# Kernel tuning notes

Measured on AMD Instinct MI355X. Metric: run time of the kernel, lower is better.

## Reference

```python
import jax, jax.numpy as jnp
import numpy as np

EPS = 1e-4
SLOPE = 0.01
NFFT = 512
HOP = 256
CH_IN = 8
CH_H = 64
FREQ = NFFT // 2 + 1
LEN = 48000
BATCH = 2


def hann(n):
    return (0.5 - 0.5 * jnp.cos(2.0 * np.pi * jnp.arange(n) / n)).astype(jnp.float32)


def stft(x):
    # x: (B, C, L) -> (B, 2, C, F, T)  (torch.stft: center=True, reflect pad, hann window)
    pad = NFFT // 2
    xp = jnp.pad(x, ((0, 0), (0, 0), (pad, pad)), mode='reflect')
    T = 1 + x.shape[-1] // HOP
    idx = jnp.arange(T)[:, None] * HOP + jnp.arange(NFFT)[None, :]
    frames = xp[..., idx] * hann(NFFT)            # (B, C, T, NFFT)
    sp = jnp.fft.rfft(frames, axis=-1)            # (B, C, T, F)
    sp = jnp.swapaxes(sp, -1, -2)                 # (B, C, F, T)
    return jnp.stack([sp.real, sp.imag], axis=1).astype(jnp.float32)


def istft(re, im, length):
    # re, im: (B, C, F, T) -> (B, C, length) via windowed overlap-add
    sp = jnp.swapaxes(re + 1j * im, -1, -2)       # (B, C, T, F)
    win = hann(NFFT)
    frames = jnp.fft.irfft(sp, n=NFFT, axis=-1) * win
    pad = NFFT // 2
    total = length + 2 * pad
    T = frames.shape[-2]
    idx = jnp.arange(T)[:, None] * HOP + jnp.arange(NFFT)[None, :]
    out = jnp.zeros(frames.shape[:-2] + (total,), frames.dtype).at[..., idx].add(frames)
    wsum = jnp.zeros((total,), frames.dtype).at[idx].add(jnp.broadcast_to(win ** 2, (T, NFFT)))
    return (out / jnp.maximum(wsum, 1e-11))[..., pad:pad + length]


def conv2d(x, w, b, padT=0):
    y = jax.lax.conv_general_dilated(x, w, (1, 1), ((0, 0), (padT, padT)),
                                     dimension_numbers=('NCHW', 'OIHW', 'NCHW'))
    return y + b[None, :, None, None]


def cconv(x, w, b, padT=0):
    # complex conv on x: (B,2,C,F,T); w: (2,O,C,kf,kt) = [W_real, W_imag]; b: (2,O)
    r = conv2d(x[:, 0], w[0], b[0], padT) - conv2d(x[:, 1], w[1], b[1], padT)
    i = conv2d(x[:, 1], w[0], b[0], padT) + conv2d(x[:, 0], w[1], b[1], padT)
    return jnp.stack([r, i], axis=1)


def modExp(x, m=5.0):
    em = float(np.exp(m))
    return jnp.where(x > m, (x - m) * em + em, jnp.exp(jnp.minimum(x, m)))


def cExp(t):
    e = modExp(t[:, 0]) - 1.0
    return jnp.stack([e * jnp.cos(t[:, 1] - 1.0), e * jnp.sin(t[:, 1] - 1.0)], axis=1)


def snap(x):
    x = jnp.where((x >= 0) & (x < EPS), EPS, x)
    return jnp.where((x < 0) & (x > -EPS), -EPS, x)


def cLog(t):
    re = snap(t[:, 0])
    im = snap(t[:, 1])
    real = jnp.log(jnp.sqrt(im ** 2 + re ** 2 + EPS ** 2) + 1.0)
    imag = jnp.arctan(im / re)
    return jnp.stack([real, imag], axis=1)


def cMul(a, b):
    r = a[:, 0] * b[:, 0] - a[:, 1] * b[:, 1]
    i = a[:, 0] * b[:, 1] + a[:, 1] * b[:, 0]
    return jnp.stack([r, i], axis=1)


def trelu(t, tr, b):
    nr = t[:, 0] * tr[0, 0] + t[:, 1] * tr[0, 1] + b[0]
    ni = t[:, 0] * tr[1, 0] + t[:, 1] * tr[1, 1] + b[1]
    return jnp.stack([jax.nn.leaky_relu(nr, SLOPE), jax.nn.leaky_relu(ni, SLOPE)], axis=1)


def tgate(t, tr, b):
    gr = jax.nn.sigmoid(t[:, 0] * tr[0, 0] + t[:, 1] * tr[0, 1] + b[0])
    gi = jax.nn.sigmoid(t[:, 0] * tr[1, 0] + t[:, 1] * tr[1, 1] + b[1])
    return gr * gi + (1.0 - gr) * (1.0 - gi)


def perm(t):
    return jnp.transpose(t, (0, 1, 3, 2, 4))


def lrelu(x):
    return jax.nn.leaky_relu(x, SLOPE)


def forward(mix, fs_w, fs_b, fr_w, fr_b, c1r_w, c1r_b, c1i_w, c1i_b, c1_w, c1_b,
            c2r_w, c2r_b, c2i_w, c2i_b, c2_w, c2_b, a1_t, a1_b, a2_t, a2_b,
            c3r_w, c3r_b, c3i_w, c3i_b, c3_w, c3_b, c4r_w, c4r_b, c4i_w, c4i_b,
            c4_w, c4_b, a3_t, a3_b, a4_t, a4_b, f1_w, f1_b, f2_w, f2_b,
            cw_w, cw_b, fg_t, fg_b):
    ts = perm(cconv(perm(stft(mix)), fs_w, fs_b))      # (B,2,C,F,T)
    # ---- branch 1 ----
    tl = cLog(ts)
    tl = jnp.stack([conv2d(tl[:, 0], c1r_w, c1r_b), conv2d(tl[:, 1], c1r_w, c1r_b)], 1)
    tl = jnp.stack([conv2d(lrelu(tl[:, 0]), c1i_w, c1i_b), conv2d(tl[:, 1], c1i_w, c1i_b)], 1)
    tl = trelu(cExp(tl), a1_t, a1_b)
    t = cconv(tl, c1_w, c1_b)
    tl = cLog(t)
    tl = jnp.stack([conv2d(tl[:, 0], c2r_w, c2r_b, 7), conv2d(tl[:, 1], c2r_w, c2r_b, 7)], 1)[..., :-7]
    tl = jnp.stack([conv2d(lrelu(tl[:, 0]), c2i_w, c2i_b, 7), conv2d(tl[:, 1], c2i_w, c2i_b, 7)], 1)[..., :-7]
    tl = cExp(tl)
    tl1 = tl
    tc = cconv(ts, c2_w, c2_b, 7)[..., :-7]
    t = trelu(cMul(tl, tc), a2_t, a2_b)
    t = cconv(t, f1_w, f1_b)
    td1 = jnp.sum(ts - t, axis=2, keepdims=True) / ts.shape[2]
    # ---- branch 2 ----
    tl = cLog(ts)
    tl = jnp.stack([conv2d(tl[:, 0], c3r_w, c3r_b), conv2d(tl[:, 1], c3r_w, c3r_b)], 1)
    tl = jnp.stack([conv2d(lrelu(tl[:, 0]), c3i_w, c3i_b), conv2d(tl[:, 1], c3i_w, c3i_b)], 1)
    tl = trelu(cExp(tl), a3_t, a3_b)
    t = cconv(tl, c3_w, c3_b)
    tl = cLog(t)
    tl = jnp.stack([conv2d(tl[:, 0], c4r_w, c4r_b, 7), conv2d(tl[:, 1], c4r_w, c4r_b, 7)], 1)[..., :-7]
    tl = jnp.stack([conv2d(lrelu(tl[:, 0]), c4i_w, c4i_b, 7), conv2d(tl[:, 1], c4i_w, c4i_b, 7)], 1)[..., :-7]
    tl = cExp(tl)
    tc = cconv(ts, c4_w, c4_b, 7)[..., :-7]
    t = trelu(cMul(tl, tc), a4_t, a4_b)
    td2 = cconv(t, f2_w, f2_b)                         # (B,2,1,F,T)
    # ---- fuse ----
    f = cconv(jnp.concatenate([tl1, tl], axis=2), cw_w, cw_b)
    f = tgate(f, fg_t, fg_b)[:, None]                  # (B,1,1,F,T)
    td = td1 * f + td2 * (1.0 - f)
    t = perm(cconv(perm(td), fr_w, fr_b))
    return istft(t[:, 0], t[:, 1], LEN)                # (B,1,LEN)


def setup_inputs() -> dict:
    ks = iter(jax.random.split(jax.random.key(0), 64))
    def rn(shape, s=0.05):
        return s * jax.random.normal(next(ks), shape, jnp.float32)
    F, C, H = FREQ, CH_IN, CH_H
    inp = {
        'mix': jax.random.normal(next(ks), (BATCH, C, LEN), jnp.float32),
        'fs_w': rn((2, F, F, 1, 1)), 'fs_b': rn((2, F), 0.01),
        'fr_w': rn((2, F, F, 1, 1)), 'fr_b': rn((2, F), 0.01),
        'c1r_w': rn((H, C, 1, 1)), 'c1r_b': rn((H,), 0.01),
        'c1i_w': rn((H, H, 1, 1)), 'c1i_b': rn((H,), 0.01),
        'c1_w': rn((2, H, H, 1, 1)), 'c1_b': rn((2, H), 0.01),
        'c2r_w': rn((H, H, 1, 8)), 'c2r_b': rn((H,), 0.01),
        'c2i_w': rn((H, H, 1, 8)), 'c2i_b': rn((H,), 0.01),
        'c2_w': rn((2, H, C, 1, 8)), 'c2_b': rn((2, H), 0.01),
        'a1_t': rn((2, 2, H, F, 1), 0.5), 'a1_b': rn((2, H, F, 1), 0.5),
        'a2_t': rn((2, 2, H, F, 1), 0.5), 'a2_b': rn((2, H, F, 1), 0.5),
        'c3r_w': rn((H, C, 1, 1)), 'c3r_b': rn((H,), 0.01),
        'c3i_w': rn((H, H, 1, 1)), 'c3i_b': rn((H,), 0.01),
        'c3_w': rn((2, H, H, 1, 1)), 'c3_b': rn((2, H), 0.01),
        'c4r_w': rn((H, H, 1, 8)), 'c4r_b': rn((H,), 0.01),
        'c4i_w': rn((H, H, 1, 8)), 'c4i_b': rn((H,), 0.01),
        'c4_w': rn((2, H, C, 1, 8)), 'c4_b': rn((2, H), 0.01),
        'a3_t': rn((2, 2, H, F, 1), 0.5), 'a3_b': rn((2, H, F, 1), 0.5),
        'a4_t': rn((2, 2, H, F, 1), 0.5), 'a4_b': rn((2, H, F, 1), 0.5),
        'f1_w': rn((2, C, H, 1, 1)), 'f1_b': rn((2, C), 0.01),
        'f2_w': rn((2, 1, H, 1, 1)), 'f2_b': rn((2, 1), 0.01),
        'cw_w': rn((2, 1, 2 * H, 1, 1)), 'cw_b': rn((2, 1), 0.01),
        'fg_t': rn((2, 2, 1, F, 1), 0.5), 'fg_b': rn((2, 1, F, 1), 0.5),
    }
    return inp


def reference(mix, fs_w, fs_b, fr_w, fr_b, c1r_w, c1r_b, c1i_w, c1i_b, c1_w, c1_b,
              c2r_w, c2r_b, c2i_w, c2i_b, c2_w, c2_b, a1_t, a1_b, a2_t, a2_b,
              c3r_w, c3r_b, c3i_w, c3i_b, c3_w, c3_b, c4r_w, c4r_b, c4i_w, c4i_b,
              c4_w, c4_b, a3_t, a3_b, a4_t, a4_b, f1_w, f1_b, f2_w, f2_b,
              cw_w, cw_b, fg_t, fg_b):
    return forward(mix, fs_w, fs_b, fr_w, fr_b, c1r_w, c1r_b, c1i_w, c1i_b, c1_w, c1_b,
                   c2r_w, c2r_b, c2i_w, c2i_b, c2_w, c2_b, a1_t, a1_b, a2_t, a2_b,
                   c3r_w, c3r_b, c3i_w, c3i_b, c3_w, c3_b, c4r_w, c4r_b, c4i_w, c4i_b,
                   c4_w, c4_b, a3_t, a3_b, a4_t, a4_b, f1_w, f1_b, f2_w, f2_b,
                   cw_w, cw_b, fg_t, fg_b)
```

## Files before the change

### kernel.cpp

```cpp
#include <hip/hip_runtime.h>
#include <math.h>

#define DEV __device__ __forceinline__

constexpr int B_   = 2;
constexpr int C_IN = 8;
constexpr int H_   = 64;
constexpr int F_   = 257;
constexpr int T_   = 188;
constexpr int TW   = 96;
constexpr int NFFT = 512;
constexpr int HOP  = 256;
constexpr int LEN  = 48000;
constexpr int PADL = 256;
constexpr int FT   = F_ * T_;
constexpr float EPSV  = 1e-4f;
constexpr float SLOPEV = 0.01f;
constexpr float PI2 = 6.283185307179586f;

typedef __attribute__((ext_vector_type(8))) short short8;
typedef __attribute__((ext_vector_type(4))) short short4v;
typedef __attribute__((ext_vector_type(4))) float float4v;

DEV float lrelu_f(float x) { return x > 0.f ? x : SLOPEV * x; }
DEV float snap_f(float x) {
  if (x >= 0.f && x < EPSV) return EPSV;
  if (x < 0.f && x > -EPSV) return -EPSV;
  return x;
}
DEV float fast_atan(float z) {
  float az = fabsf(z);
  float u = az > 1.f ? __builtin_amdgcn_rcpf(az) : az;
  float u2 = u * u;
  float p = -0.01172120f;
  p = p * u2 + 0.05265332f;
  p = p * u2 - 0.11643287f;
  p = p * u2 + 0.19354346f;
  p = p * u2 - 0.33262347f;
  p = p * u2 + 0.99997726f;
  float r = p * u;
  if (az > 1.f) r = 1.5707963267948966f - r;
  return z < 0.f ? -r : r;
}
DEV float modexp_f(float x) {
  const float em = 148.4131591025766f;
  return x > 5.f ? (x - 5.f) * em + em : __expf(x);
}
DEV void cexp_f(float tr, float ti, float& er, float& ei) {
  float e = modexp_f(tr) - 1.f;
  float a = ti - 1.f;
  er = e * __cosf(a); ei = e * __sinf(a);
}
DEV float sigmoid_f(float x) { return 1.f / (1.f + __expf(-x)); }

DEV short f2bf(float x) {
  unsigned u = __float_as_uint(x);
  unsigned r = (u + 0x7fffu + ((u >> 16) & 1u)) >> 16;
  return (short)r;
}
DEV float bf2f(short h) {
  return __uint_as_float(((unsigned)(unsigned short)h) << 16);
}
DEV unsigned pack_hl(float v) {
  short hi = f2bf(v);
  short lo = f2bf(v - bf2f(hi));
  return ((unsigned)(unsigned short)hi << 16) | (unsigned)(unsigned short)lo;
}

__global__ void k_mixsplit(const float* __restrict__ x, short* __restrict__ hi,
                           short* __restrict__ lo) {
  int i = blockIdx.x * 256 + threadIdx.x;
  if (i >= B_ * C_IN * LEN / 4) return;
  float4v v = *(const float4v*)(x + (size_t)i * 4);
  short4v h, l;
  #pragma unroll
  for (int j = 0; j < 4; ++j) {
    h[j] = f2bf(v[j]);
    l[j] = f2bf(v[j] - bf2f(h[j]));
  }
  *(short4v*)(hi + (size_t)i * 4) = h;
  *(short4v*)(lo + (size_t)i * 4) = l;
}

__global__ __launch_bounds__(256) void k_mixdft(const float* __restrict__ W,
                                                short* __restrict__ wpk) {
  constexpr int MT = 33;
  __shared__ float wr_s[F_], wi_s[F_];
  int m = blockIdx.x;
  int k = blockIdx.y * 256 + threadIdx.x;
  int po = m >= F_;
  int fo = m - po * F_;
  if (m < 2 * F_) {
    for (int i = threadIdx.x; i < F_; i += 256) {
      wr_s[i] = W[fo * F_ + i];
      wi_s[i] = W[F_ * F_ + fo * F_ + i];
    }
  }
  __syncthreads();
  float val = 0.f;
  if (m < 2 * F_) {
    float sd, cd;
    sincosf((PI2 / NFFT) * k, &sd, &cd);
    float cs = 1.f, sn = 0.f;
    float ar = 0.f, ai = 0.f;
    for (int fi = 0; fi < F_; ++fi) {
      float wrv = wr_s[fi], wiv = wi_s[fi];
      ar += wrv * cs + wiv * sn;
      ai += wiv * cs - wrv * sn;
      float t2 = cs * cd - sn * sd;
      sn = sn * cd + cs * sd;
      cs = t2;
    }
    float win = 0.5f - 0.5f * cd;
    val = (po ? ai : ar) * win;
  }
  int mtg = m >> 4;
  int lane2 = ((k >> 3) & 3) * 16 + (m & 15);
  int s = k >> 5;
  int j = k & 7;
  short hi = f2bf(val);
  short lo = f2bf(val - bf2f(hi));
  wpk[(((0 * 16 + s) * MT + mtg) * 64 + lane2) * 8 + j] = hi;
  wpk[(((16 + s) * MT + mtg) * 64 + lane2) * 8 + j] = lo;
}

constexpr int TWS = 48;
__global__ __launch_bounds__(256) void k_stftmix(
    const short* __restrict__ mhi, const short* __restrict__ mlo,
    const short* __restrict__ wpk, const float* __restrict__ bias,
    float* __restrict__ Y) {
  constexpr int PITCH = 136;
  constexpr int MT = 33;
  __shared__ short xs_hi[TWS * PITCH];
  __shared__ short xs_lo[TWS * PITCH];
  int mg = blockIdx.x;
  int bc = blockIdx.y;
  int b = bc >> 3, c = bc & 7;
  int t0 = blockIdx.z * TWS;
  int tid = threadIdx.x;
  int lane = tid & 63;
  int wv = __builtin_amdgcn_readfirstlane(tid >> 6);
  int mtg = mg * 4 + wv;
  int q = lane >> 4;
  int n = lane & 15;

  const short* mh_ = mhi + (size_t)(b * C_IN + c) * LEN;
  const short* ml_ = mlo + (size_t)(b * C_IN + c) * LEN;

  float4v acc[3];
  #pragma unroll
  for (int nt = 0; nt < 3; ++nt) acc[nt] = (float4v)(0.f);

  const short8* wp = (const short8*)wpk;
  for (int round = 0; round < 4; ++round) {
    if (round) __syncthreads();
    for (int i = tid; i < TWS * 16; i += 256) {
      int tl = i >> 4, u = i & 15;
      int kk0 = u * 8;
      int t = t0 + tl;
      int g0 = t * HOP + round * 128 + kk0 - PADL;
      short8 h, l;
      if (t < T_ && g0 >= 0 && g0 + 7 < LEN) {
        h = *(const short8*)(mh_ + g0);
        l = *(const short8*)(ml_ + g0);
      } else {
        #pragma unroll
        for (int j = 0; j < 8; ++j) {
          short hv = 0, lv = 0;
          if (t < T_) {
            int g = g0 + j;
            if (g < 0) g = -g;
            if (g >= LEN) g = 2 * LEN - 2 - g;
            hv = mh_[g]; lv = ml_[g];
          }
          h[j] = hv; l[j] = lv;
        }
      }
      *(short8*)&xs_hi[tl * PITCH + kk0] = h;
      *(short8*)&xs_lo[tl * PITCH + kk0] = l;
    }
    __syncthreads();
    #pragma unroll
    for (int s2 = 0; s2 < 4; ++s2) {
      int s = round * 4 + s2;
      short8 Ah, Al;
      if (mtg < MT) {
        Ah = wp[((0 * 16 + s) * MT + mtg) * 64 + lane];
        Al = wp[((16 + s) * MT + mtg) * 64 + lane];
      }
      short8 Bh[3], Bl[3];
      #pragma unroll
      for (int nt = 0; nt < 3; ++nt) {
        int off = (nt * 16 + n) * PITCH + s2 * 32 + q * 8;
        Bh[nt] = *(const short8*)&xs_hi[off];
        Bl[nt] = *(const short8*)&xs_lo[off];
      }
      if (mtg < MT) {
        #pragma unroll
        for (int nt = 0; nt < 3; ++nt) {
          acc[nt] = __builtin_amdgcn_mfma_f32_16x16x32_bf16(Ah, Bh[nt], acc[nt], 0, 0, 0);
          acc[nt] = __builtin_amdgcn_mfma_f32_16x16x32_bf16(Ah, Bl[nt], acc[nt], 0, 0, 0);
          acc[nt] = __builtin_amdgcn_mfma_f32_16x16x32_bf16(Al, Bh[nt], acc[nt], 0, 0, 0);
        }
      }
    }
  }

  if (mtg < MT) {
    #pragma unroll
    for (int nt = 0; nt < 3; ++nt) {
      int t = t0 + nt * 16 + n;
      if (t >= T_) continue;
      #pragma unroll
      for (int r = 0; r < 4; ++r) {
        int m = mtg * 16 + q * 4 + r;
        if (m >= 2 * F_) continue;
        int po = m >= F_;
        int fo = m - po * F_;
        float badd = po ? bias[fo] + bias[F_ + fo] : bias[fo] - bias[F_ + fo];
        Y[((size_t)((b * 2 + po) * C_IN + c)) * FT + fo * T_ + t] = acc[nt][r] + badd;
      }
    }
  }
}

template<int CH>
__global__ void k_fmix(const float* __restrict__ X, const float* __restrict__ W,
                       const float* __restrict__ bias, float* __restrict__ Y) {
  int fo = blockIdx.x;
  int bc = blockIdx.y; int c = bc % CH; int b = bc / CH;
  int t = threadIdx.x;
  if (t >= T_) return;
  const float* wr = W + fo * F_;
  const float* wi = W + F_ * F_ + fo * F_;
  const float* xr = X + ((b * 2 + 0) * CH + c) * FT + t;
  const float* xi = X + ((b * 2 + 1) * CH + c) * FT + t;
  float ar = 0.f, ai = 0.f;
  for (int fi = 0; fi < F_; ++fi) {
    float wrv = wr[fi], wiv = wi[fi];
    float xrv = xr[fi * T_], xiv = xi[fi * T_];
    ar += wrv * xrv - wiv * xiv;
    ai += wrv * xiv + wiv * xrv;
  }
  float br = bias[fo], bi = bias[F_ + fo];
  Y[((b * 2 + 0) * CH + c) * FT + fo * T_ + t] = ar + br - bi;
  Y[((b * 2 + 1) * CH + c) * FT + fo * T_ + t] = ai + br + bi;
}

template<int CIN, int K>
DEV void repack_real_body(const float* __restrict__ W, short* __restrict__ wpk, int i) {
  constexpr int CC = (CIN >= 32) ? (CIN / 32) : 1;
  constexpr int NSTEP = (CIN * K + 31) / 32;
  int total = 2 * NSTEP * 4 * 64 * 8;
  if (i >= total) return;
  int j = i & 7;
  int lane = (i >> 3) & 63;
  int mt = (i >> 9) & 3;
  int s = (i >> 11) % NSTEP;
  int split = i / (NSTEP * 2048);
  int q = lane >> 4;
  int m = mt * 16 + (lane & 15);
  int tap = s / CC;
  int c = (s % CC) * 32 + q * 8 + j;
  float w = 0.f;
  if (c < CIN && tap < K) w = W[(m * CIN + c) * K + tap];
  short hi = f2bf(w);
  wpk[i] = split ? f2bf(w - bf2f(hi)) : hi;
}

template<int CIN2, int COUT2, int K>
DEV void repack_cplx_body(const float* __restrict__ W, short* __restrict__ wpk, int i) {
  constexpr int CIN = CIN2 / 2, COUT = COUT2 / 2;
  constexpr int NSTEP = CIN2 * K / 32;
  constexpr int MT = (COUT2 + 15) / 16;
  int total = 2 * NSTEP * MT * 64 * 8;
  if (i >= total) return;
  int j = i & 7;
  int lane = (i >> 3) & 63;
  int idx = i >> 9;
  int mt = idx % MT; idx /= MT;
  int s = idx % NSTEP;
  int split = idx / NSTEP;
  int q = lane >> 4;
  int m = mt * 16 + (lane & 15);
  int tap, pi, ci;
  if constexpr (CIN2 == 128) {
    tap = 0;
    int cs = s * 32 + q * 8 + j;
    int half = cs / 64, r = cs % 64;
    ci = half * 32 + r / 2;
    pi = r & 1;
  } else {
    tap = s * 2 + (q >> 1);
    int cs = (q & 1) * 8 + j;
    pi = cs / CIN;
    ci = cs % CIN;
  }
  float w = 0.f;
  if (m < COUT2) {
    int po = m / COUT, ho = m % COUT;
    float wr = W[((0 * COUT + ho) * CIN + ci) * K + tap];
    float wi = W[((1 * COUT + ho) * CIN + ci) * K + tap];
    w = (po == pi) ? wr : (po == 0 ? -wi : wi);
  }
  short hi = f2bf(w);
  wpk[i] = split ? f2bf(w - bf2f(hi)) : hi;
}

__global__ __launch_bounds__(256) void k_repack_all(
    const float* c1r_w, const float* c1i_w, const float* c2r_w, const float* c2i_w,
    const float* c3r_w, const float* c3i_w, const float* c4r_w, const float* c4i_w,
    const float* c1_w, const float* c2_w, const float* c3_w, const float* c4_w,
    const float* f1_w, const float* f2_w,
    short* o0, short* o1, short* o2, short* o3, short* o4, short* o5, short* o6,
    short* o7, short* o8, short* o9, short* o10, short* o11, short* o12, short* o13) {
  int i = blockIdx.x * 256 + threadIdx.x;
  switch (blockIdx.y) {
    case 0:  repack_real_body<C_IN, 1>(c1r_w, o0, i); break;
    case 1:  repack_real_body<H_,   1>(c1i_w, o1, i); break;
    case 2:  repack_real_body<H_,   8>(c2r_w, o2, i); break;
    case 3:  repack_real_body<H_,   8>(c2i_w, o3, i); break;
    case 4:  repack_real_body<C_IN, 1>(c3r_w, o4, i); break;
    case 5:  repack_real_body<H_,   1>(c3i_w, o5, i); break;
    case 6:  repack_real_body<H_,   8>(c4r_w, o6, i); break;
    case 7:  repack_real_body<H_,   8>(c4i_w, o7, i); break;
    case 8:  repack_cplx_body<128, 128, 1>(c1_w, o8, i); break;
    case 9:  repack_cplx_body<16,  128, 8>(c2_w, o9, i); break;
    case 10: repack_cplx_body<128, 128, 1>(c3_w, o10, i); break;
    case 11: repack_cplx_body<16,  128, 8>(c4_w, o11, i); break;
    case 12: repack_cplx_body<128, 16,  1>(f1_w, o12, i); break;
    case 13: repack_cplx_body<128, 2,   1>(f2_w, o13, i); break;
  }
}

template<int CIN, int K, int PRO, int EPI>
__global__ __launch_bounds__(256) void k_conv_mfma(
    const float* __restrict__ Xa, const float* __restrict__ Xb,
    const short* __restrict__ wpka, const short* __restrict__ wpkb,
    const float* __restrict__ biasa, const float* __restrict__ biasb,
    float* __restrict__ Ya, float* __restrict__ Yb) {
  constexpr int CC = (CIN >= 32) ? (CIN / 32) : 1;
  constexpr int NSTEP = (CIN * K + 31) / 32;
  constexpr int PITCH = 72;
  constexpr int ROWS = TW + (K - 1);
  __shared__ short xs_hi[ROWS * PITCH];
  __shared__ short xs_lo[ROWS * PITCH];
  int f = blockIdx.x;
  int y = blockIdx.y;
  int brsel = (y >= B_ * 2);
  int bp = y - brsel * (B_ * 2);
  int p = bp & 1; int b = bp >> 1;
  const float* X = brsel ? Xb : Xa;
  const short* wpk = brsel ? wpkb : wpka;
  const float* bias = brsel ? biasb : biasa;
  float* Y = brsel ? Yb : Ya;
  int t0 = blockIdx.z * TW;
  int tid = threadIdx.x;

  {
    int lo_inval = (K - 1) - t0;
    if (lo_inval < 0) lo_inval = 0;
    int hi_start = T_ - t0 + (K - 1);
    if (hi_start > ROWS) hi_start = ROWS;
    for (int i = tid; i < lo_inval * PITCH; i += 256) { xs_hi[i] = 0; xs_lo[i] = 0; }
    int nhi = (ROWS - hi_start) * PITCH;
    for (int i = tid; i < nhi; i += 256) {
      int o = hi_start * PITCH + i;
      xs_hi[o] = 0; xs_lo[o] = 0;
    }
    if (CIN < 32) {
      constexpr int BAND = 32 - ((CIN < 32) ? CIN : 32);
      for (int i = tid; i < ROWS * BAND; i += 256) {
        int rr = i / BAND, c = CIN + i % BAND;
        xs_hi[rr * PITCH + c] = 0; xs_lo[rr * PITCH + c] = 0;
      }
    }
  }
  __syncthreads();

  const float* Xr_ = X + (size_t)((b * 2 + 0) * CIN) * FT + f * T_;
  const float* Xi_ = X + (size_t)((b * 2 + 1) * CIN) * FT + f * T_;
  const float* Xp  = X + (size_t)((b * 2 + p) * CIN) * FT + f * T_;
  const unsigned* Xu = (const unsigned*)X + (size_t)((b * 2 + p) * CIN) * FT + f * T_;
  {
    constexpr int STEP_C = 256 / ROWS, STEP_R = 256 % ROWS;
    int c = tid / ROWS;
    int rr = tid - c * ROWS;
    while (c < CIN) {
      int t = t0 + rr - (K - 1);
      if (t >= 0 && t < T_) {
        short hi, lo;
        if (PRO == 3) {
          unsigned v = Xu[c * FT + t];
          hi = (short)(v >> 16);
          lo = (short)(v & 0xffffu);
        } else {
          float v;
          if (PRO == 2) {
            float re = snap_f(Xr_[c * FT + t]);
            float im = snap_f(Xi_[c * FT + t]);
            v = (p == 0) ? __logf(sqrtf(im * im + re * re + EPSV * EPSV) + 1.f)
                         : fast_atan(im / re);
          } else {
            v = Xp[c * FT + t];
            if (PRO == 1 && p == 0) v = lrelu_f(v);
          }
          hi = f2bf(v);
          lo = f2bf(v - bf2f(hi));
        }
        xs_hi[rr * PITCH + c] = hi;
        xs_lo[rr * PITCH + c] = lo;
      }
      rr += STEP_R; c += STEP_C;
      if (rr >= ROWS) { rr -= ROWS; c += 1; }
    }
  }
  __syncthreads();

  int lane = tid & 63;
  int wv = __builtin_amdgcn_readfirstlane(tid >> 6);
  int mh = wv >> 1;
  int tc = wv & 1;
  int q = lane >> 4;
  int n = lane & 15;
  int wbase = tc * 48;

  float4v acc[2][3];
  #pragma unroll
  for (int mt = 0; mt < 2; ++mt)
    #pragma unroll
    for (int nt = 0; nt < 3; ++nt) acc[mt][nt] = (float4v)(0.f);

  const short8* wp = (const short8*)wpk;
  #pragma unroll
  for (int s = 0; s < NSTEP; ++s) {
    int tap = s / CC;
    int c0 = (s % CC) * 32;
    short8 Ah[2], Al[2];
    #pragma unroll
    for (int mt = 0; mt < 2; ++mt) {
      int mtg = mh * 2 + mt;
      Ah[mt] = wp[((0 * NSTEP + s) * 4 + mtg) * 64 + lane];
      Al[mt] = wp[((1 * NSTEP + s) * 4 + mtg) * 64 + lane];
    }
    short8 Bh[3], Bl[3];
    #pragma unroll
    for (int nt = 0; nt < 3; ++nt) {
      int off = (wbase + nt * 16 + n + tap) * PITCH + c0 + q * 8;
      Bh[nt] = *(const short8*)&xs_hi[off];
      Bl[nt] = *(const short8*)&xs_lo[off];
    }
    #pragma unroll
    for (int mt = 0; mt < 2; ++mt) {
      #pragma unroll
      for (int nt = 0; nt < 3; ++nt) {
        acc[mt][nt] = __builtin_amdgcn_mfma_f32_16x16x32_bf16(Ah[mt], Bh[nt], acc[mt][nt], 0, 0, 0);
        acc[mt][nt] = __builtin_amdgcn_mfma_f32_16x16x32_bf16(Ah[mt], Bl[nt], acc[mt][nt], 0, 0, 0);
        acc[mt][nt] = __builtin_amdgcn_mfma_f32_16x16x32_bf16(Al[mt], Bh[nt], acc[mt][nt], 0, 0, 0);
      }
    }
  }

  float* Yp = Y + (size_t)((b * 2 + p) * H_) * FT + f * T_;
  unsigned* Yu = (unsigned*)Y + (size_t)((b * 2 + p) * H_) * FT + f * T_;
  #pragma unroll
  for (int nt = 0; nt < 3; ++nt) {
    int t = t0 + wbase + nt * 16 + n;
    if (t >= T_) continue;
    #pragma unroll
    for (int mt = 0; mt < 2; ++mt) {
      #pragma unroll
      for (int r = 0; r < 4; ++r) {
        int h = (mh * 2 + mt) * 16 + q * 4 + r;
        float v = acc[mt][nt][r] + bias[h];
        if (EPI == 0) {
          Yp[h * FT + t] = v;
        } else {
          if (EPI == 1 && p == 0) v = lrelu_f(v);
          Yu[h * FT + t] = pack_hl(v);
        }
      }
    }
  }
}

template<int COUT2, int PRO>
__global__ __launch_bounds__(256) void k_cconv128(
    const float* __restrict__ X0a, const float* __restrict__ X1a,
    const float* __restrict__ X0b, const float* __restrict__ X1b,
    const short* __restrict__ wpka, const short* __restrict__ wpkb,
    const float* __restrict__ ata, const float* __restrict__ atb,
    const float* __restrict__ aba, const float* __restrict__ abb,
    const float* __restrict__ biasa, const float* __restrict__ biasb,
    float* __restrict__ Ya, float* __restrict__ Yb) {
  constexpr int MT = (COUT2 + 15) / 16;
  constexpr int MTW = (MT > 4) ? 4 : MT;
  constexpr int COUT = COUT2 / 2;
  constexpr int NSTEP = 4;
  constexpr int PITCH = 72;
  __shared__ short xs_hi[TW * PITCH];
  __shared__ short xs_lo[TW * PITCH];
  __shared__ float coef[6][64];
  int f = blockIdx.x;
  int y = blockIdx.y;
  int brsel = (y >= B_);
  int b = y - brsel * B_;
  const float* X0 = brsel ? X0b : X0a;
  const float* X1 = brsel ? X1b : X1a;
  const short* wpk = brsel ? wpkb : wpka;
  const float* at = brsel ? atb : ata;
  const float* ab = brsel ? abb : aba;
  const float* bias = brsel ? biasb : biasa;
  float* Y = brsel ? Yb : Ya;
  int t0 = blockIdx.z * TW;
  int tid = threadIdx.x;
  int lane = tid & 63;
  int wv = __builtin_amdgcn_readfirstlane(tid >> 6);
  int mh = wv >> 1;
  int tc = wv & 1;
  int q = lane >> 4;
  int n = lane & 15;
  int wbase = tc * 48;

  if (tid < 64) {
    int h = tid;
    coef[0][h] = at[(0 * H_ + h) * F_ + f];
    coef[1][h] = at[(1 * H_ + h) * F_ + f];
    coef[2][h] = at[(2 * H_ + h) * F_ + f];
    coef[3][h] = at[(3 * H_ + h) * F_ + f];
    coef[4][h] = ab[h * F_ + f];
    coef[5][h] = ab[(H_ + h) * F_ + f];
  }
  {
    int inval0 = T_ - t0;
    if (inval0 < 0) inval0 = 0;
    if (inval0 > TW) inval0 = TW;
    int nfill = (TW - inval0) * PITCH;
    for (int i = tid; i < nfill; i += 256) {
      int o = inval0 * PITCH + i;
      xs_hi[o] = 0; xs_lo[o] = 0;
    }
  }

  const float* b0r = X0 + (size_t)((b * 2 + 0) * H_) * FT + f * T_;
  const float* b0i = X0 + (size_t)((b * 2 + 1) * H_) * FT + f * T_;
  const float* b1r = X1 + (size_t)((b * 2 + 0) * H_) * FT + f * T_;
  const float* b1i = X1 + (size_t)((b * 2 + 1) * H_) * FT + f * T_;

  float4v acc[MTW][3];
  #pragma unroll
  for (int mt = 0; mt < MTW; ++mt)
    #pragma unroll
    for (int nt = 0; nt < 3; ++nt) acc[mt][nt] = (float4v)(0.f);

  const short8* wp = (const short8*)wpk;
  for (int half = 0; half < 2; ++half) {
    __syncthreads();
    for (int i = tid; i < 32 * TW; i += 256) {
      int hh = i / TW, tl = i % TW;
      int t = t0 + tl;
      if (t >= T_) continue;
      int h = half * 32 + hh;
      float xr = b0r[h * FT + t], xi = b0i[h * FT + t];
      float vr, vi;
      if (PRO == 1) {
        float er, ei;
        cexp_f(xr, xi, er, ei);
        vr = lrelu_f(er * coef[0][h] + ei * coef[1][h] + coef[4][h]);
        vi = lrelu_f(er * coef[2][h] + ei * coef[3][h] + coef[5][h]);
      } else {
        float yr = b1r[h * FT + t], yi = b1i[h * FT + t];
        float mr = xr * yr - xi * yi;
        float mi = xr * yi + xi * yr;
        vr = lrelu_f(mr * coef[0][h] + mi * coef[1][h] + coef[4][h]);
        vi = lrelu_f(mr * coef[2][h] + mi * coef[3][h] + coef[5][h]);
      }
      int cs0 = hh * 2, cs1 = hh * 2 + 1;
      short hr = f2bf(vr), hi2 = f2bf(vi);
      xs_hi[tl * PITCH + cs0] = hr;
      xs_lo[tl * PITCH + cs0] = f2bf(vr - bf2f(hr));
      xs_hi[tl * PITCH + cs1] = hi2;
      xs_lo[tl * PITCH + cs1] = f2bf(vi - bf2f(hi2));
    }
    __syncthreads();
    #pragma unroll
    for (int s2 = 0; s2 < 2; ++s2) {
      int s = half * 2 + s2;
      short8 Bh[3], Bl[3];
      #pragma unroll
      for (int nt = 0; nt < 3; ++nt) {
        int off = (wbase + nt * 16 + n) * PITCH + s2 * 32 + q * 8;
        Bh[nt] = *(const short8*)&xs_hi[off];
        Bl[nt] = *(const short8*)&xs_lo[off];
      }
      #pragma unroll
      for (int mt = 0; mt < MTW; ++mt) {
        int mtg = mh * 4 + mt;
        if (mtg >= MT) continue;
        short8 Ah = wp[((0 * NSTEP + s) * MT + mtg) * 64 + lane];
        short8 Al = wp[((1 * NSTEP + s) * MT + mtg) * 64 + lane];
        #pragma unroll
        for (int nt = 0; nt < 3; ++nt) {
          acc[mt][nt] = __builtin_amdgcn_mfma_f32_16x16x32_bf16(Ah, Bh[nt], acc[mt][nt], 0, 0, 0);
          acc[mt][nt] = __builtin_amdgcn_mfma_f32_16x16x32_bf16(Ah, Bl[nt], acc[mt][nt], 0, 0, 0);
          acc[mt][nt] = __builtin_amdgcn_mfma_f32_16x16x32_bf16(Al, Bh[nt], acc[mt][nt], 0, 0, 0);
        }
      }
    }
  }

  float* Yp = Y + (size_t)b * COUT2 * FT + f * T_;
  #pragma unroll
  for (int nt = 0; nt < 3; ++nt) {
    int t = t0 + wbase + nt * 16 + n;
    if (t >= T_) continue;
    #pragma unroll
    for (int mt = 0; mt < MTW; ++mt) {
      int mtg = mh * 4 + mt;
      if (mtg >= MT) continue;
      #pragma unroll
      for (int r = 0; r < 4; ++r) {
        int o2 = mtg * 16 + q * 4 + r;
        if (o2 >= COUT2) continue;
        int po = o2 / COUT, ho = o2 % COUT;
        float br2 = bias[ho], bi2 = bias[COUT + ho];
        float badd = (po == 0) ? br2 - bi2 : br2 + bi2;
        Yp[o2 * FT + t] = acc[mt][nt][r] + badd;
      }
    }
  }
}

__global__ __launch_bounds__(256) void k_cconv16(
    const float* __restrict__ Xa, const float* __restrict__ Xb,
    const short* __restrict__ wpka, const short* __restrict__ wpkb,
    const float* __restrict__ biasa, const float* __restrict__ biasb,
    float* __restrict__ Ya, float* __restrict__ Yb) {
  constexpr int MT = 8, NSTEP = 4, PITCH = 24, ROWS = TW + 7, COUT = 64, COUT2 = 128;
  __shared__ short xs_hi[ROWS * PITCH];
  __shared__ short xs_lo[ROWS * PITCH];
  int f = blockIdx.x;
  int y = blockIdx.y;
  int brsel = (y >= B_);
  int b = y - brsel * B_;
  const float* X = brsel ? Xb : Xa;
  const short* wpk = brsel ? wpkb : wpka;
  const float* bias = brsel ? biasb : biasa;
  float* Y = brsel ? Yb : Ya;
  int t0 = blockIdx.z * TW;
  int tid = threadIdx.x;

  {
    int lo_inval = 7 - t0;
    if (lo_inval < 0) lo_inval = 0;
    int hi_start = T_ - t0 + 7;
    if (hi_start > ROWS) hi_start = ROWS;
    for (int i = tid; i < lo_inval * PITCH; i += 256) { xs_hi[i] = 0; xs_lo[i] = 0; }
    int nhi = (ROWS - hi_start) * PITCH;
    for (int i = tid; i < nhi; i += 256) {
      int o = hi_start * PITCH + i;
      xs_hi[o] = 0; xs_lo[o] = 0;
    }
  }
  __syncthreads();

  const float* Xp = X + (size_t)b * 16 * FT + f * T_;
  for (int i = tid; i < 16 * ROWS; i += 256) {
    int c = i / ROWS, rr = i % ROWS;
    int t = t0 + rr - 7;
    if (t < 0 || t >= T_) continue;
    float v = Xp[c * FT + t];
    short hi = f2bf(v);
    short lo = f2bf(v - bf2f(hi));
    xs_hi[rr * PITCH + c] = hi;
    xs_lo[rr * PITCH + c] = lo;
  }
  __syncthreads();

  int lane = tid & 63;
  int wv = __builtin_amdgcn_readfirstlane(tid >> 6);
  int mh = wv >> 1;
  int tc = wv & 1;
  int q = lane >> 4;
  int n = lane & 15;
  int wbase = tc * 48;

  float4v acc[4][3];
  #pragma unroll
  for (int mt = 0; mt < 4; ++mt)
    #pragma unroll
    for (int nt = 0; nt < 3; ++nt) acc[mt][nt] = (float4v)(0.f);

  const short8* wp = (const short8*)wpk;
  #pragma unroll
  for (int s = 0; s < NSTEP; ++s) {
    int tap = s * 2 + (q >> 1);
    int coff = (q & 1) * 8;
    short8 Bh[3], Bl[3];
    #pragma unroll
    for (int nt = 0; nt < 3; ++nt) {
      int off = (wbase + nt * 16 + n + tap) * PITCH + coff;
      Bh[nt] = *(const short8*)&xs_hi[off];
      Bl[nt] = *(const short8*)&xs_lo[off];
    }
    #pragma unroll
    for (int mt = 0; mt < 4; ++mt) {
      int mtg = mh * 4 + mt;
      short8 Ah = wp[((0 * NSTEP + s) * MT + mtg) * 64 + lane];
      short8 Al = wp[((1 * NSTEP + s) * MT + mtg) * 64 + lane];
      #pragma unroll
      for (int nt = 0; nt < 3; ++nt) {
        acc[mt][nt] = __builtin_amdgcn_mfma_f32_16x16x32_bf16(Ah, Bh[nt], acc[mt][nt], 0, 0, 0);
        acc[mt][nt] = __builtin_amdgcn_mfma_f32_16x16x32_bf16(Ah, Bl[nt], acc[mt][nt], 0, 0, 0);
        acc[mt][nt] = __builtin_amdgcn_mfma_f32_16x16x32_bf16(Al, Bh[nt], acc[mt][nt], 0, 0, 0);
      }
    }
  }

  float* Yp = Y + (size_t)b * COUT2 * FT + f * T_;
  #pragma unroll
  for (int nt = 0; nt < 3; ++nt) {
    int t = t0 + wbase + nt * 16 + n;
    if (t >= T_) continue;
    #pragma unroll
    for (int mt = 0; mt < 4; ++mt) {
      #pragma unroll
      for (int r = 0; r < 4; ++r) {
        int o2 = (mh * 4 + mt) * 16 + q * 4 + r;
        int po = o2 / COUT, ho = o2 % COUT;
        float br2 = bias[ho], bi2 = bias[COUT + ho];
        float badd = (po == 0) ? br2 - bi2 : br2 + bi2;
        Yp[o2 * FT + t] = acc[mt][nt][r] + badd;
      }
    }
  }
}

__global__ void k_cexp_pk(const unsigned* __restrict__ Xa, const unsigned* __restrict__ Xb,
                          float* __restrict__ Ya, float* __restrict__ Yb) {
  int i = blockIdx.x * blockDim.x + threadIdx.x;
  if (i >= 2 * B_ * H_ * FT) return;
  int brsel = (i >= B_ * H_ * FT);
  int j = i - brsel * (B_ * H_ * FT);
  const unsigned* X = brsel ? Xb : Xa;
  float* Y = brsel ? Yb : Ya;
  int b = j / (H_ * FT);
  int r = j % (H_ * FT);
  size_t i0 = (size_t)(b * 2) * H_ * FT + r;
  size_t i1 = i0 + (size_t)H_ * FT;
  unsigned v0 = X[i0], v1 = X[i1];
  float tr = bf2f((short)(v0 >> 16)) + bf2f((short)(v0 & 0xffffu));
  float ti = bf2f((short)(v1 >> 16)) + bf2f((short)(v1 & 0xffffu));
  float er, ei;
  cexp_f(tr, ti, er, ei);
  Y[i0] = er;
  Y[i1] = ei;
}

__global__ void k_td1(const float* __restrict__ ts, const float* __restrict__ t8,
                      float* __restrict__ td1) {
  int i = blockIdx.x * blockDim.x + threadIdx.x;
  if (i >= B_ * 2 * FT) return;
  int bp = i / FT; int r = i % FT;
  const float* a = ts + bp * C_IN * FT + r;
  const float* c2 = t8 + bp * C_IN * FT + r;
  float acc = 0.f;
  #pragma unroll
  for (int c = 0; c < C_IN; ++c) acc += a[c * FT] - c2[c * FT];
  td1[i] = acc * (1.f / C_IN);
}

__global__ void k_fuse(const float* __restrict__ tl1, const float* __restrict__ tl2,
                       const float* __restrict__ td1, const float* __restrict__ td2,
                       const float* __restrict__ cw, const float* __restrict__ cwb,
                       const float* __restrict__ fgt, const float* __restrict__ fgb,
                       float* __restrict__ td) {
  int i = blockIdx.x * blockDim.x + threadIdx.x;
  if (i >= B_ * FT) return;
  int b = i / FT; int r = i % FT; int f = r / T_;
  const float* x1r = tl1 + (b * 2) * H_ * FT + r;
  const float* x1i = x1r + H_ * FT;
  const float* x2r = tl2 + (b * 2) * H_ * FT + r;
  const float* x2i = x2r + H_ * FT;
  float fr = 0.f, fi = 0.f;
  for (int c = 0; c < H_; ++c) {
    float w1r = cw[c], w2r = cw[H_ + c], w1i = cw[2 * H_ + c], w2i = cw[3 * H_ + c];
    float a1r = x1r[c * FT], a1i = x1i[c * FT];
    float a2r = x2r[c * FT], a2i = x2i[c * FT];
    fr += w1r * a1r - w1i * a1i + w2r * a2r - w2i * a2i;
    fi += w1r * a1i + w1i * a1r + w2r * a2i + w2i * a2r;
  }
  fr += cwb[0] - cwb[1];
  fi += cwb[0] + cwb[1];
  float t00 = fgt[f], t01 = fgt[F_ + f], t10 = fgt[2 * F_ + f], t11 = fgt[3 * F_ + f];
  float gr = sigmoid_f(fr * t00 + fi * t01 + fgb[f]);
  float gi = sigmoid_f(fr * t10 + fi * t11 + fgb[F_ + f]);
  float gg = gr * gi + (1.f - gr) * (1.f - gi);
  int i0 = (b * 2) * FT + r, i1 = i0 + FT;
  td[i0] = td1[i0] * gg + td2[i0] * (1.f - gg);
  td[i1] = td1[i1] * gg + td2[i1] * (1.f - gg);
}

__global__ __launch_bounds__(320) void k_iframes(const float* __restrict__ sp,
                                                 float* __restrict__ frames) {
  __shared__ float Xr[F_], Xi[F_];
  int blk = blockIdx.x;
  int t = blk % T_;
  int b = blk / T_;
  int tid = threadIdx.x;
  for (int i = tid; i < F_; i += 320) {
    Xr[i] = sp[(b * 2 + 0) * FT + i * T_ + t];
    Xi[i] = sp[(b * 2 + 1) * FT + i * T_ + t];
  }
  __syncthreads();
  int n = tid;
  if (n <= 256) {
    float sd, cd;
    sincosf((PI2 / NFFT) * n, &sd, &cd);
    float cs = cd, sn = sd;
    float ac = 0.f, as = 0.f;
    for (int f = 1; f < 256; ++f) {
      ac += Xr[f] * cs;
      as += Xi[f] * sn;
      float t2 = cs * cd - sn * sd;
      sn = sn * cd + cs * sd;
      cs = t2;
    }
    float base = Xr[0] + Xr[256] * (1.f - 2.f * (n & 1));
    float win = 0.5f - 0.5f * cd;
    float scale = win * (1.f / NFFT);
    float* fr = frames + (size_t)(b * T_ + t) * NFFT;
    fr[n] = (base + 2.f * ac - 2.f * as) * scale;
    if (n >= 1 && n <= 255)
      fr[NFFT - n] = (base + 2.f * ac + 2.f * as) * scale;
  }
}

__global__ void k_ola(const float* __restrict__ frames, float* __restrict__ out) {
  int i = blockIdx.x * blockDim.x + threadIdx.x;
  if (i >= B_ * LEN) return;
  int b = i / LEN; int j = i % LEN;
  int p = j + PADL;
  int t0 = p / HOP; int n0 = p - t0 * HOP;
  float acc = 0.f, wsum = 0.f;
  if (t0 < T_) {
    acc += frames[(b * T_ + t0) * NFFT + n0];
    float w = 0.5f - 0.5f * __cosf((PI2 / NFFT) * n0);
    wsum += w * w;
  }
  int t1 = t0 - 1, n1 = n0 + HOP;
  if (t1 >= 0 && t1 < T_) {
    acc += frames[(b * T_ + t1) * NFFT + n1];
    float w = 0.5f - 0.5f * __cosf((PI2 / NFFT) * n1);
    wsum += w * w;
  }
  out[i] = acc / fmaxf(wsum, 1e-11f);
}

extern "C" void kernel_launch(void* const* d_in, const int* in_sizes, int n_in,
                              void* d_out, int out_size, void* d_ws, size_t ws_size,
                              hipStream_t stream) {
  const float* mix   = (const float*)d_in[0];
  const float* fs_w  = (const float*)d_in[1];
  const float* fs_b  = (const float*)d_in[2];
  const float* fr_w  = (const float*)d_in[3];
  const float* fr_b  = (const float*)d_in[4];
  const float* c1r_w = (const float*)d_in[5];
  const float* c1r_b = (const float*)d_in[6];
  const float* c1i_w = (const float*)d_in[7];
  const float* c1i_b = (const float*)d_in[8];
  const float* c1_w  = (const float*)d_in[9];
  const float* c1_b  = (const float*)d_in[10];
  const float* c2r_w = (const float*)d_in[11];
  const float* c2r_b = (const float*)d_in[12];
  const float* c2i_w = (const float*)d_in[13];
  const float* c2i_b = (const float*)d_in[14];
  const float* c2_w  = (const float*)d_in[15];
  const float* c2_b  = (const float*)d_in[16];
  const float* a1_t  = (const float*)d_in[17];
  const float* a1_b  = (const float*)d_in[18];
  const float* a2_t  = (const float*)d_in[19];
  const float* a2_b  = (const float*)d_in[20];
  const float* c3r_w = (const float*)d_in[21];
  const float* c3r_b = (const float*)d_in[22];
  const float* c3i_w = (const float*)d_in[23];
  const float* c3i_b = (const float*)d_in[24];
  const float* c3_w  = (const float*)d_in[25];
  const float* c3_b  = (const float*)d_in[26];
  const float* c4r_w = (const float*)d_in[27];
  const float* c4r_b = (const float*)d_in[28];
  const float* c4i_w = (const float*)d_in[29];
  const float* c4i_b = (const float*)d_in[30];
  const float* c4_w  = (const float*)d_in[31];
  const float* c4_b  = (const float*)d_in[32];
  const float* a3_t  = (const float*)d_in[33];
  const float* a3_b  = (const float*)d_in[34];
  const float* a4_t  = (const float*)d_in[35];
  const float* a4_b  = (const float*)d_in[36];
  const float* f1_w  = (const float*)d_in[37];
  const float* f1_b  = (const float*)d_in[38];
  const float* f2_w  = (const float*)d_in[39];
  const float* f2_b  = (const float*)d_in[40];
  const float* cw_w  = (const float*)d_in[41];
  const float* cw_b  = (const float*)d_in[42];
  const float* fg_t  = (const float*)d_in[43];
  const float* fg_b  = (const float*)d_in[44];

  const size_t S8 = (size_t)B_ * 2 * C_IN * FT;
  const size_t SH = (size_t)B_ * 2 * H_ * FT;
  const size_t S1 = (size_t)B_ * 2 * FT;
  float* ws  = (float*)d_ws;
  float* ts0 = ws;
  float* ts  = ts0 + S8;
  float* A1  = ts + S8;
  float* A2  = A1 + SH;
  float* Bb  = A2 + SH;
  float* Cc  = Bb + SH;
  float* td1 = Cc + SH;
  float* td2 = td1 + S1;
  float* tdf = td2 + S1;
  float* tdr = tdf + S1;
  float* s8  = ts0;
  float* frames = ts0;

  short* wtail = (short*)(tdr + S1);
  constexpr int SZ_C8K1   = 2 * 1  * 4 * 64 * 8;
  constexpr int SZ_C64K1  = 2 * 2  * 4 * 64 * 8;
  constexpr int SZ_C64K8  = 2 * 16 * 4 * 64 * 8;
  constexpr int SZ_CC128  = 2 * 4  * 8 * 64 * 8;
  constexpr int SZ_CF     = 2 * 4  * 1 * 64 * 8;
  constexpr int SZ_SM     = 2 * 16 * 33 * 64 * 8;
  short* w_c1r = wtail;
  short* w_c1i = w_c1r + SZ_C8K1;
  short* w_c2r = w_c1i + SZ_C64K1;
  short* w_c2i = w_c2r + SZ_C64K8;
  short* w_c3r = w_c2i + SZ_C64K8;
  short* w_c3i = w_c3r + SZ_C8K1;
  short* w_c4r = w_c3i + SZ_C64K1;
  short* w_c4i = w_c4r + SZ_C64K8;
  short* w_cc1 = w_c4i + SZ_C64K8;
  short* w_cc2 = w_cc1 + SZ_CC128;
  short* w_cc3 = w_cc2 + SZ_CC128;
  short* w_cc4 = w_cc3 + SZ_CC128;
  short* w_cf1 = w_cc4 + SZ_CC128;
  short* w_cf2 = w_cf1 + SZ_CF;
  short* w_sm  = w_cf2 + SZ_CF;
  short* mhi   = w_sm + SZ_SM;
  short* mlo   = mhi + (size_t)B_ * C_IN * LEN;

  const int nH = B_ * H_ * FT;
  const int nP = B_ * FT;
  const dim3 mrgrid(F_, 2 * B_ * 2, 2);
  const dim3 mcgrid(F_, 2 * B_, 2);
  const dim3 cgrid(F_, B_, 2);

  k_repack_all<<<dim3(256, 14), 256, 0, stream>>>(
      c1r_w, c1i_w, c2r_w, c2i_w, c3r_w, c3i_w, c4r_w, c4i_w,
      c1_w, c2_w, c3_w, c4_w, f1_w, f2_w,
      w_c1r, w_c1i, w_c2r, w_c2i, w_c3r, w_c3i, w_c4r, w_c4i,
      w_cc1, w_cc2, w_cc3, w_cc4, w_cf1, w_cf2);

  k_mixsplit<<<(B_ * C_IN * LEN / 4 + 255) / 256, 256, 0, stream>>>(mix, mhi, mlo);
  k_mixdft<<<dim3(528, 2), 256, 0, stream>>>(fs_w, w_sm);
  k_stftmix<<<dim3(9, 16, 4), 256, 0, stream>>>(mhi, mlo, w_sm, fs_b, ts);

  k_conv_mfma<C_IN, 1, 2, 1><<<mrgrid, 256, 0, stream>>>(
      ts, ts, w_c1r, w_c3r, c1r_b, c3r_b, A1, A2);
  k_conv_mfma<H_, 1, 3, 0><<<mrgrid, 256, 0, stream>>>(
      A1, A2, w_c1i, w_c3i, c1i_b, c3i_b, Bb, Cc);
  k_cconv128<128, 1><<<mcgrid, 256, 0, stream>>>(
      Bb, Bb, Cc, Cc, w_cc1, w_cc3, a1_t, a3_t, a1_b, a3_b,
      c1_b, c3_b, A1, A2);
  k_conv_mfma<H_, 8, 2, 1><<<mrgrid, 256, 0, stream>>>(
      A1, A2, w_c2r, w_c4r, c2r_b, c4r_b, Bb, Cc);
  k_conv_mfma<H_, 8, 3, 2><<<mrgrid, 256, 0, stream>>>(
      Bb, Cc, w_c2i, w_c4i, c2i_b, c4i_b, A1, A2);
  k_cexp_pk<<<(2 * nH + 255) / 256, 256, 0, stream>>>(
      (const unsigned*)A1, (const unsigned*)A2, Bb, Cc);
  k_cconv16<<<mcgrid, 256, 0, stream>>>(
      ts, ts, w_cc2, w_cc4, c2_b, c4_b, A1, A2);
  k_cconv128<16, 2><<<cgrid, 256, 0, stream>>>(
      Bb, A1, Bb, A1, w_cf1, w_cf1, a2_t, a2_t, a2_b, a2_b,
      f1_b, f1_b, s8, s8);
  k_td1<<<(B_ * 2 * FT + 255) / 256, 256, 0, stream>>>(ts, s8, td1);
  k_cconv128<2, 2><<<cgrid, 256, 0, stream>>>(
      Cc, A2, Cc, A2, w_cf2, w_cf2, a4_t, a4_t, a4_b, a4_b,
      f2_b, f2_b, td2, td2);

  k_fuse<<<(nP + 255) / 256, 256, 0, stream>>>(Bb, Cc, td1, td2, cw_w, cw_b, fg_t, fg_b, tdf);
  k_fmix<1><<<dim3(F_, B_), 192, 0, stream>>>(tdf, fr_w, fr_b, tdr);
  k_iframes<<<B_ * T_, 320, 0, stream>>>(tdr, frames);
  k_ola<<<(B_ * LEN + 255) / 256, 256, 0, stream>>>(frames, (float*)d_out);
}
```

Baseline: 771.2 us.

## Fold final frequency mix into inverse DFT matrix and run it on MFMA

The final complex frequency-mixing layer (fr_w) is multiplied into the windowed inverse real DFT at run time, giving one 512x514 matrix plus a folded bias vector. The matrix is stored as split bf16 hi/lo pairs. The per-frame inverse DFT and the separate scalar fmix kernel are replaced by one MFMA kernel that multiplies this matrix by the spectrum tile using three bf16 products. This removes a launch and the scalar FMA loops, but adds a per-call weight-folding kernel that loops over 257 frequencies for every matrix entry.

After: 797.4 us. 1.03x slower.

```diff
diff --git a/kernel.cpp b/kernel.cpp
--- a/kernel.cpp
+++ b/kernel.cpp
@@ -66,6 +66,9 @@
   short lo = f2bf(v - bf2f(hi));
   return ((unsigned)(unsigned short)hi << 16) | (unsigned)(unsigned short)lo;
 }
+DEV float unpack_hl(unsigned v) {
+  return bf2f((short)(v >> 16)) + bf2f((short)(v & 0xffffu));
+}
 
 __global__ void k_mixsplit(const float* __restrict__ x, short* __restrict__ hi,
                            short* __restrict__ lo) {
@@ -122,6 +125,59 @@
   short lo = f2bf(val - bf2f(hi));
   wpk[(((0 * 16 + s) * MT + mtg) * 64 + lane2) * 8 + j] = hi;
   wpk[(((16 + s) * MT + mtg) * 64 + lane2) * 8 + j] = lo;
+}
+
+__global__ __launch_bounds__(288) void k_rmixdft(const float* __restrict__ W,
+                                                 const float* __restrict__ bias,
+                                                 short* __restrict__ wpk,
+                                                 float* __restrict__ fb) {
+  constexpr int MT2 = 32, NST = 17;
+  int nrow = blockIdx.x;
+  int k = blockIdx.y * 288 + threadIdx.x;
+  float sd, cd;
+  sincosf((PI2 / NFFT) * nrow, &sd, &cd);
+  float scale = (0.5f - 0.5f * cd) * (1.f / NFFT);
+  if (k < NST * 32) {
+    float acc = 0.f;
+    if (k < 2 * F_) {
+      int p = k >= F_;
+      int fi = k - p * F_;
+      const float* wr = W + fi;
+      const float* wi = W + (size_t)F_ * F_ + fi;
+      float cs = 1.f, sn = 0.f;
+      for (int f = 0; f < F_; ++f) {
+        float cf = (f == 0 || f == 256) ? 1.f : 2.f;
+        float Crv = scale * cf * cs;
+        float Civ = (f == 0 || f == 256) ? 0.f : (-scale * 2.f * sn);
+        float wrv = wr[(size_t)f * F_], wiv = wi[(size_t)f * F_];
+        acc += (p == 0) ? (Crv * wrv + Civ * wiv) : (Civ * wrv - Crv * wiv);
+        float t2 = cs * cd - sn * sd;
+        sn = sn * cd + cs * sd;
+        cs = t2;
+      }
+    }
+    int mtg = nrow >> 4;
+    int lane2 = ((k >> 3) & 3) * 16 + (nrow & 15);
+    int s = k >> 5;
+    int j = k & 7;
+    short hi = f2bf(acc);
+    short lo = f2bf(acc - bf2f(hi));
+    wpk[(((0 * NST + s) * MT2 + mtg) * 64 + lane2) * 8 + j] = hi;
+    wpk[(((NST + s) * MT2 + mtg) * 64 + lane2) * 8 + j] = lo;
+  } else if (k == NST * 32) {
+    float cs = 1.f, sn = 0.f, acc = 0.f;
+    for (int f = 0; f < F_; ++f) {
+      float cf = (f == 0 || f == 256) ? 1.f : 2.f;
+      float Crv = scale * cf * cs;
+      float Civ = (f == 0 || f == 256) ? 0.f : (-scale * 2.f * sn);
+      float brf = bias[f], bif = bias[F_ + f];
+      acc += Crv * (brf - bif) + Civ * (brf + bif);
+      float t2 = cs * cd - sn * sd;
+      sn = sn * cd + cs * sd;
+      cs = t2;
+    }
+    fb[nrow] = acc;
+  }
 }
 
 constexpr int TWS = 48;
@@ -224,27 +280,83 @@
   }
 }
 
-template<int CH>
-__global__ void k_fmix(const float* __restrict__ X, const float* __restrict__ W,
-                       const float* __restrict__ bias, float* __restrict__ Y) {
-  int fo = blockIdx.x;
-  int bc = blockIdx.y; int c = bc % CH; int b = bc / CH;
-  int t = threadIdx.x;
-  if (t >= T_) return;
-  const float* wr = W + fo * F_;
-  const float* wi = W + F_ * F_ + fo * F_;
-  const float* xr = X + ((b * 2 + 0) * CH + c) * FT + t;
-  const float* xi = X + ((b * 2 + 1) * CH + c) * FT + t;
-  float ar = 0.f, ai = 0.f;
-  for (int fi = 0; fi < F_; ++fi) {
-    float wrv = wr[fi], wiv = wi[fi];
-    float xrv = xr[fi * T_], xiv = xi[fi * T_];
-    ar += wrv * xrv - wiv * xiv;
-    ai += wrv * xiv + wiv * xrv;
-  }
-  float br = bias[fo], bi = bias[F_ + fo];
-  Y[((b * 2 + 0) * CH + c) * FT + fo * T_ + t] = ar + br - bi;
-  Y[((b * 2 + 1) * CH + c) * FT + fo * T_ + t] = ai + br + bi;
+__global__ __launch_bounds__(256) void k_istftmix(
+    const float* __restrict__ X, const short* __restrict__ wpk,
+    const float* __restrict__ fb, float* __restrict__ frames) {
+  constexpr int PITCH = 136;
+  constexpr int MT2 = 32, NST = 17;
+  __shared__ short xs_hi[TWS * PITCH];
+  __shared__ short xs_lo[TWS * PITCH];
+  int mg = blockIdx.x;
+  int b = blockIdx.y;
+  int t0 = blockIdx.z * TWS;
+  int tid = threadIdx.x;
+  int lane = tid & 63;
+  int wv = __builtin_amdgcn_readfirstlane(tid >> 6);
+  int mtg = mg * 4 + wv;
+  int q = lane >> 4;
+  int n = lane & 15;
+
+  float4v acc[3];
+  #pragma unroll
+  for (int nt = 0; nt < 3; ++nt) acc[nt] = (float4v)(0.f);
+
+  const short8* wp = (const short8*)wpk;
+  for (int round = 0; round < 5; ++round) {
+    if (round) __syncthreads();
+    for (int i = tid; i < TWS * 16; i += 256) {
+      int tl = i >> 4, u = i & 15;
+      int kk0 = u * 8;
+      int t = t0 + tl;
+      short8 h, l;
+      #pragma unroll
+      for (int j = 0; j < 8; ++j) {
+        int kg = round * 128 + kk0 + j;
+        float v = 0.f;
+        if (t < T_ && kg < 2 * F_) {
+          int p = kg >= F_;
+          int fi = kg - p * F_;
+          v = X[((size_t)(b * 2 + p)) * FT + fi * T_ + t];
+        }
+        short hv = f2bf(v);
+        h[j] = hv;
+        l[j] = f2bf(v - bf2f(hv));
+      }
+      *(short8*)&xs_hi[tl * PITCH + kk0] = h;
+      *(short8*)&xs_lo[tl * PITCH + kk0] = l;
+    }
+    __syncthreads();
+    int ns = (round < 4) ? 4 : 1;
+    for (int s2 = 0; s2 < ns; ++s2) {
+      int s = round * 4 + s2;
+      short8 Ah = wp[((0 * NST + s) * MT2 + mtg) * 64 + lane];
+      short8 Al = wp[((1 * NST + s) * MT2 + mtg) * 64 + lane];
+      short8 Bh[3], Bl[3];
+      #pragma unroll
+      for (int nt = 0; nt < 3; ++nt) {
+        int off = (nt * 16 + n) * PITCH + s2 * 32 + q * 8;
+        Bh[nt] = *(const short8*)&xs_hi[off];
+        Bl[nt] = *(const short8*)&xs_lo[off];
+      }
+      #pragma unroll
+      for (int nt = 0; nt < 3; ++nt) {
+        acc[nt] = __builtin_amdgcn_mfma_f32_16x16x32_bf16(Ah, Bh[nt], acc[nt], 0, 0, 0);
+        acc[nt] = __builtin_amdgcn_mfma_f32_16x16x32_bf16(Ah, Bl[nt], acc[nt], 0, 0, 0);
+        acc[nt] = __builtin_amdgcn_mfma_f32_16x16x32_bf16(Al, Bh[nt], acc[nt], 0, 0, 0);
+      }
+    }
+  }
+
+  #pragma unroll
+  for (int nt = 0; nt < 3; ++nt) {
+    int t = t0 + nt * 16 + n;
+    if (t >= T_) continue;
+    #pragma unroll
+    for (int r = 0; r < 4; ++r) {
+      int m = mtg * 16 + q * 4 + r;
+      frames[((size_t)(b * T_ + t)) * NFFT + m] = acc[nt][r] + fb[m];
+    }
+  }
 }
 
 template<int CIN, int K>
@@ -749,8 +861,8 @@
   size_t i0 = (size_t)(b * 2) * H_ * FT + r;
   size_t i1 = i0 + (size_t)H_ * FT;
   unsigned v0 = X[i0], v1 = X[i1];
-  float tr = bf2f((short)(v0 >> 16)) + bf2f((short)(v0 & 0xffffu));
-  float ti = bf2f((short)(v1 >> 16)) + bf2f((short)(v1 & 0xffffu));
+  float tr = unpack_hl(v0);
+  float ti = unpack_hl(v1);
   float er, ei;
   cexp_f(tr, ti, er, ei);
   Y[i0] = er;
@@ -799,41 +911,6 @@
   int i0 = (b * 2) * FT + r, i1 = i0 + FT;
   td[i0] = td1[i0] * gg + td2[i0] * (1.f - gg);
   td[i1] = td1[i1] * gg + td2[i1] * (1.f - gg);
-}
-
-__global__ __launch_bounds__(320) void k_iframes(const float* __restrict__ sp,
-                                                 float* __restrict__ frames) {
-  __shared__ float Xr[F_], Xi[F_];
-  int blk = blockIdx.x;
-  int t = blk % T_;
-  int b = blk / T_;
-  int tid = threadIdx.x;
-  for (int i = tid; i < F_; i += 320) {
-    Xr[i] = sp[(b * 2 + 0) * FT + i * T_ + t];
-    Xi[i] = sp[(b * 2 + 1) * FT + i * T_ + t];
-  }
-  __syncthreads();
-  int n = tid;
-  if (n <= 256) {
-    float sd, cd;
-    sincosf((PI2 / NFFT) * n, &sd, &cd);
-    float cs = cd, sn = sd;
-    float ac = 0.f, as = 0.f;
-    for (int f = 1; f < 256; ++f) {
-      ac += Xr[f] * cs;
-      as += Xi[f] * sn;
-      float t2 = cs * cd - sn * sd;
-      sn = sn * cd + cs * sd;
-      cs = t2;
-    }
-    float base = Xr[0] + Xr[256] * (1.f - 2.f * (n & 1));
-    float win = 0.5f - 0.5f * cd;
-    float scale = win * (1.f / NFFT);
-    float* fr = frames + (size_t)(b * T_ + t) * NFFT;
-    fr[n] = (base + 2.f * ac - 2.f * as) * scale;
-    if (n >= 1 && n <= 255)
-      fr[NFFT - n] = (base + 2.f * ac + 2.f * as) * scale;
-  }
 }
 
 __global__ void k_ola(const float* __restrict__ frames, float* __restrict__ out) {
@@ -930,6 +1007,7 @@
   constexpr int SZ_CC128  = 2 * 4  * 8 * 64 * 8;
   constexpr int SZ_CF     = 2 * 4  * 1 * 64 * 8;
   constexpr int SZ_SM     = 2 * 16 * 33 * 64 * 8;
+  constexpr int SZ_SM2    = 2 * 17 * 32 * 64 * 8;
   short* w_c1r = wtail;
   short* w_c1i = w_c1r + SZ_C8K1;
   short* w_c2r = w_c1i + SZ_C64K1;
@@ -947,6 +1025,8 @@
   short* w_sm  = w_cf2 + SZ_CF;
   short* mhi   = w_sm + SZ_SM;
   short* mlo   = mhi + (size_t)B_ * C_IN * LEN;
+  short* w_sm2 = mlo + (size_t)B_ * C_IN * LEN;
+  float* fb    = (float*)(w_sm2 + SZ_SM2);
 
   const int nH = B_ * H_ * FT;
   const int nP = B_ * FT;
@@ -962,6 +1042,7 @@
 
   k_mixsplit<<<(B_ * C_IN * LEN / 4 + 255) / 256, 256, 0, stream>>>(mix, mhi, mlo);
   k_mixdft<<<dim3(528, 2), 256, 0, stream>>>(fs_w, w_sm);
+  k_rmixdft<<<dim3(512, 2), 288, 0, stream>>>(fr_w, fr_b, w_sm2, fb);
   k_stftmix<<<dim3(9, 16, 4), 256, 0, stream>>>(mhi, mlo, w_sm, fs_b, ts);
 
   k_conv_mfma<C_IN, 1, 2, 1><<<mrgrid, 256, 0, stream>>>(
@@ -988,7 +1069,6 @@
       f2_b, f2_b, td2, td2);
 
   k_fuse<<<(nP + 255) / 256, 256, 0, stream>>>(Bb, Cc, td1, td2, cw_w, cw_b, fg_t, fg_b, tdf);
-  k_fmix<1><<<dim3(F_, B_), 192, 0, stream>>>(tdf, fr_w, fr_b, tdr);
-  k_iframes<<<B_ * T_, 320, 0, stream>>>(tdr, frames);
+  k_istftmix<<<dim3(8, B_, 4), 256, 0, stream>>>(tdf, w_sm2, fb, frames);
   k_ola<<<(B_ * LEN + 255) / 256, 256, 0, stream>>>(frames, (float*)d_out);
 }
```
